# Kernel optimization log

Measured on AMD Instinct MI355X. Metric: run time of the kernel, lower is better.

Reference implementation:

```python
import jax, jax.numpy as jnp
import numpy as np

B, S, D, H, NUM_LABELS = 16, 1024, 1024, 16, 3
LN_EPS = 1e-5


def setup_inputs() -> dict:
    key = jax.random.key(0)
    ks = iter(jax.random.split(key, 16))

    def w(shape, k):
        return jax.random.normal(k, shape, jnp.float32) * 0.02

    inp = {}
    inp["embedded"] = jax.random.normal(next(ks), (B, S, D), jnp.float32)
    inp["attention_mask"] = jnp.ones((B, S), jnp.float32)
    for pfx in ("p2h", "h2p"):
        for name in ("q", "k", "v", "o"):
            inp[f"{pfx}_W{name}"] = w((D, D), next(ks))
            inp[f"{pfx}_b{name}"] = jnp.zeros((D,), jnp.float32)
        inp[f"{pfx}_ln_g"] = jnp.ones((D,), jnp.float32)
        inp[f"{pfx}_ln_b"] = jnp.zeros((D,), jnp.float32)
    inp["W1"] = w((4 * D, D), next(ks)); inp["b1"] = jnp.zeros((D,), jnp.float32)
    inp["W2"] = w((D, D // 2), next(ks)); inp["b2"] = jnp.zeros((D // 2,), jnp.float32)
    inp["W3"] = w((D // 2, NUM_LABELS), next(ks)); inp["b3"] = jnp.zeros((NUM_LABELS,), jnp.float32)
    return inp


def _layernorm(x, g, b):
    mu = jnp.mean(x, axis=-1, keepdims=True)
    var = jnp.mean(jnp.square(x - mu), axis=-1, keepdims=True)
    return (x - mu) / jnp.sqrt(var + LN_EPS) * g + b


def _cross_attn(q_in, kv_in, kv_mask, Wq, bq, Wk, bk, Wv, bv, Wo, bo, g, bln):
    Bs, Sq, Dm = q_in.shape
    Sk = kv_in.shape[1]
    hd = Dm // H
    Q = (q_in @ Wq + bq).reshape(Bs, Sq, H, hd)
    K = (kv_in @ Wk + bk).reshape(Bs, Sk, H, hd)
    V = (kv_in @ Wv + bv).reshape(Bs, Sk, H, hd)
    scores = jnp.einsum("bqhd,bkhd->bhqk", Q, K) / jnp.sqrt(jnp.float32(hd))
    scores = jnp.where(kv_mask[:, None, None, :] == 0, jnp.float32(-1e9), scores)
    wts = jax.nn.softmax(scores, axis=-1)  # dropout is identity in eval
    att = jnp.einsum("bhqk,bkhd->bqhd", wts, V).reshape(Bs, Sq, Dm)
    return _layernorm(att @ Wo + bo + q_in, g, bln)


def _pool(x, m):
    s = jnp.sum(x * m[:, :, None], axis=1)
    d = jnp.clip(jnp.sum(m, axis=1, keepdims=True), 1e-9, None)
    return s / d


def reference(embedded, attention_mask,
              p2h_Wq, p2h_bq, p2h_Wk, p2h_bk, p2h_Wv, p2h_bv, p2h_Wo, p2h_bo, p2h_ln_g, p2h_ln_b,
              h2p_Wq, h2p_bq, h2p_Wk, h2p_bk, h2p_Wv, h2p_bv, h2p_Wo, h2p_bo, h2p_ln_g, h2p_ln_b,
              W1, b1, W2, b2, W3, b3):
    half = embedded.shape[1] // 2
    premise, hypothesis = embedded[:, :half], embedded[:, half:]
    pm, hm = attention_mask[:, :half], attention_mask[:, half:]
    p2h = _cross_attn(premise, hypothesis, hm,
                      p2h_Wq, p2h_bq, p2h_Wk, p2h_bk, p2h_Wv, p2h_bv, p2h_Wo, p2h_bo, p2h_ln_g, p2h_ln_b)
    h2p = _cross_attn(hypothesis, premise, pm,
                      h2p_Wq, h2p_bq, h2p_Wk, h2p_bk, h2p_Wv, h2p_bv, h2p_Wo, h2p_bo, h2p_ln_g, h2p_ln_b)
    feats = jnp.concatenate([_pool(premise, pm), _pool(hypothesis, hm),
                             _pool(p2h, pm), _pool(h2p, hm)], axis=-1)
    h1 = jax.nn.relu(feats @ W1 + b1)
    h2 = jax.nn.relu(h1 @ W2 + b2)
    return h2 @ W3 + b3
```

## Files before the change

kernel.cpp:

```cpp
#include <hip/hip_runtime.h>
#include <hip/hip_bf16.h>

typedef __attribute__((ext_vector_type(8))) __bf16 bf16x8;
typedef __attribute__((ext_vector_type(4))) float f32x4;
typedef __attribute__((ext_vector_type(4))) int i32x4;
typedef __attribute__((ext_vector_type(4))) unsigned short u16x4;

#define MFMA16(a, b, c) __builtin_amdgcn_mfma_f32_16x16x32_bf16((a), (b), (c), 0, 0, 0)

__device__ __forceinline__ void gload_lds16(const void* g, void* l)
{
    __builtin_amdgcn_global_load_lds(
        (const __attribute__((address_space(1))) unsigned int*)g,
        (__attribute__((address_space(3))) unsigned int*)l, 16, 0, 0);
}

__global__ __launch_bounds__(256) void cast_emb_kernel(const float* __restrict__ emb,
                                                       __bf16* __restrict__ Pb,
                                                       __bf16* __restrict__ Hb)
{
    int i = (blockIdx.x * 256 + threadIdx.x) * 4;
    int r = i >> 10, d = i & 1023;
    size_t src = ((size_t)(r >> 9) * 1024 + (r & 511)) * 1024 + d;
    f32x4 p = *(const f32x4*)(emb + src);
    f32x4 h = *(const f32x4*)(emb + src + 512 * 1024);
    union { __bf16 b[4]; u16x4 u; } cp, ch;
#pragma unroll
    for (int j = 0; j < 4; ++j) { cp.b[j] = (__bf16)p[j]; ch.b[j] = (__bf16)h[j]; }
    *(u16x4*)(Pb + i) = cp.u;
    *(u16x4*)(Hb + i) = ch.u;
}

struct WPtrs { const float* p[8]; };
__global__ __launch_bounds__(256) void cast_wt_kernel(WPtrs wp, __bf16* __restrict__ Wt0)
{
    const float* W = wp.p[blockIdx.z];
    __bf16* Wt = Wt0 + (size_t)blockIdx.z * 1048576;
    __shared__ float tile[32][33];
    int n0 = blockIdx.x * 32, k0 = blockIdx.y * 32;
    int tx = threadIdx.x, ty = threadIdx.y;
#pragma unroll
    for (int i = ty; i < 32; i += 8)
        tile[i][tx] = W[(size_t)(k0 + i) * 1024 + n0 + tx];
    __syncthreads();
#pragma unroll
    for (int i = ty; i < 32; i += 8)
        Wt[(size_t)(n0 + i) * 1024 + k0 + tx] = (__bf16)tile[tx][i];
}

template <int EPI>
__global__ __launch_bounds__(256, 3) void gemm_bt(const __bf16* __restrict__ A,
                                                  const __bf16* __restrict__ Bt,
                                                  const float* __restrict__ bias,
                                                  const float* __restrict__ bias2,
                                                  __bf16* __restrict__ Cb,
                                                  __bf16* __restrict__ Cb2,
                                                  float* __restrict__ Cf,
                                                  const float* __restrict__ resid,
                                                  int resid_half, int M, int N, int K)
{
    __shared__ __align__(16) __bf16 As[128 * 32];
    __shared__ __align__(16) __bf16 Bs[128 * 32];
    const int t = threadIdx.x;
    const int l = t & 63, w = t >> 6;
    const int wr = w >> 1, wc = w & 1;
    const int lrow = l & 15, lk = l >> 4;
    const int m0 = blockIdx.y * 128, n0 = blockIdx.x * 128;
    const int r0 = t >> 2, kc0 = (t & 3) * 8;

    const __bf16* gA0 = A + (size_t)(m0 + r0) * K + kc0;
    const __bf16* gA1 = gA0 + (size_t)64 * K;
    const __bf16* gB0 = Bt + (size_t)(n0 + r0) * K + kc0;
    const __bf16* gB1 = gB0 + (size_t)64 * K;
    __bf16* dA0 = &As[r0 * 32 + kc0];
    __bf16* dA1 = &As[(r0 + 64) * 32 + kc0];
    __bf16* dB0 = &Bs[r0 * 32 + kc0];
    __bf16* dB1 = &Bs[(r0 + 64) * 32 + kc0];

    const f32x4 zero = {0.f, 0.f, 0.f, 0.f};
    f32x4 acc[4][4];
#pragma unroll
    for (int mi = 0; mi < 4; ++mi)
#pragma unroll
        for (int ni = 0; ni < 4; ++ni) acc[mi][ni] = zero;

    const int nk = K >> 5;
    for (int kt = 0; kt < nk; ++kt) {
        const int ko = kt * 32;
        gload_lds16(gA0 + ko, dA0);
        gload_lds16(gA1 + ko, dA1);
        gload_lds16(gB0 + ko, dB0);
        gload_lds16(gB1 + ko, dB1);
        __syncthreads();
        bf16x8 af[4], bfv[4];
#pragma unroll
        for (int mi = 0; mi < 4; ++mi)
            af[mi] = *(const bf16x8*)(&As[(wr * 64 + mi * 16 + lrow) * 32 + lk * 8]);
#pragma unroll
        for (int ni = 0; ni < 4; ++ni)
            bfv[ni] = *(const bf16x8*)(&Bs[(wc * 64 + ni * 16 + lrow) * 32 + lk * 8]);
#pragma unroll
        for (int mi = 0; mi < 4; ++mi)
#pragma unroll
            for (int ni = 0; ni < 4; ++ni)
                acc[mi][ni] = MFMA16(af[mi], bfv[ni], acc[mi][ni]);
        __syncthreads();
    }

#pragma unroll
    for (int mi = 0; mi < 4; ++mi) {
#pragma unroll
        for (int ni = 0; ni < 4; ++ni) {
            int col = n0 + wc * 64 + ni * 16 + lrow;
            float bv = (EPI == 3 && col >= 1024) ? bias2[col - 1024] : bias[col];
#pragma unroll
            for (int r = 0; r < 4; ++r) {
                int row = m0 + wr * 64 + mi * 16 + lk * 4 + r;
                float v = acc[mi][ni][r] + bv;
                if (EPI == 0) {
                    Cb[(size_t)row * N + col] = (__bf16)v;
                } else if (EPI == 3) {
                    if (col < 1024) {
                        Cb[(size_t)row * 1024 + col] = (__bf16)v;
                    } else {
                        int c2 = col - 1024;
                        int b_ = row >> 9, pos = row & 511;
                        int h_ = c2 >> 6, hd = c2 & 63;
                        Cb2[(((size_t)(b_ * 16 + h_) * 64 + hd) << 9) + pos] = (__bf16)v;
                    }
                } else {
                    int b_ = row >> 9, s = row & 511;
                    float rv = resid[((size_t)b_ * 1024 + resid_half + s) * 1024 + col];
                    Cf[(size_t)row * N + col] = v + rv;
                }
            }
        }
    }
}

__global__ __launch_bounds__(256, 3) void attn_kernel(const __bf16* __restrict__ Q,
                                                      const __bf16* __restrict__ Kb,
                                                      const __bf16* __restrict__ Vt,
                                                      const float* __restrict__ mask,
                                                      int mask_half,
                                                      __bf16* __restrict__ att)
{
    __shared__ __align__(16) __bf16 KP[256 * 64];
    __shared__ __align__(16) float msk[512];
    const int bh = blockIdx.x, b = bh >> 4, h = bh & 15;
    const int q0 = blockIdx.y * 64;
    const int t = threadIdx.x, l = t & 63, w = t >> 6;
    const int lrow = l & 15, lk = l >> 4;
    char* KPc = (char*)KP;

    const __bf16* kbase = Kb + ((size_t)b * 512) * 1024 + h * 64;
    const __bf16* vsrc = Vt + (size_t)bh * 64 * 512;

#pragma unroll
    for (int i = 0; i < 8; ++i) {
        int c = t + i * 256;
        int pos = c >> 3, gslot = (c & 7) ^ (pos & 7);
        gload_lds16(kbase + (size_t)pos * 1024 + gslot * 8, KPc + c * 16);
    }
    for (int i = t; i < 512; i += 256) msk[i] = mask[b * 1024 + mask_half + i];

    const int qrow = q0 + w * 16 + lrow;
    const __bf16* qptr = Q + ((size_t)(b * 512 + qrow)) * 1024 + h * 64;
    bf16x8 qf0 = *(const bf16x8*)(qptr + lk * 8);
    bf16x8 qf1 = *(const bf16x8*)(qptr + 32 + lk * 8);

    const f32x4 zero = {0.f, 0.f, 0.f, 0.f};
    f32x4 av[4];
#pragma unroll
    for (int ni = 0; ni < 4; ++ni) av[ni] = zero;
    float m_run = -3e38f, su = 0.f;
    const int psw = lrow & 7;
    char* prowp = KPc + (w * 16 + lrow) * 512;
    f32x4 sc[16];

    auto qk_tile = [&]() {
#pragma unroll
        for (int jj = 0; jj < 16; ++jj) {
            const char* kb = KPc + (jj * 16 + lrow) * 128;
            bf16x8 k0 = *(const bf16x8*)(kb + ((lk ^ psw) << 4));
            bf16x8 k1 = *(const bf16x8*)(kb + (((lk + 4) ^ psw) << 4));
            f32x4 c = zero;
            c = MFMA16(k0, qf0, c);
            c = MFMA16(k1, qf1, c);
            sc[jj] = c;
        }
    };

    auto process_tile = [&](int koff) {
        float mt = -3e38f;
#pragma unroll
        for (int jj = 0; jj < 16; ++jj) {
            f32x4 mv = *(const f32x4*)(&msk[koff + jj * 16 + lk * 4]);
#pragma unroll
            for (int r = 0; r < 4; ++r) {
                float s = sc[jj][r] * 0.125f;
                if (mv[r] == 0.f) s = -1e9f;
                sc[jj][r] = s;
                mt = fmaxf(mt, s);
            }
        }
        mt = fmaxf(mt, __shfl_xor(mt, 16));
        mt = fmaxf(mt, __shfl_xor(mt, 32));
        float m_new = fmaxf(m_run, mt);
        float f = __expf(m_run - m_new);
        float ssum = 0.f;
#pragma unroll
        for (int jj = 0; jj < 16; ++jj)
#pragma unroll
            for (int r = 0; r < 4; ++r) {
                float e = __expf(sc[jj][r] - m_new);
                sc[jj][r] = e;
                ssum += e;
            }
        ssum += __shfl_xor(ssum, 16);
        ssum += __shfl_xor(ssum, 32);
        su = su * f + ssum;
        m_run = m_new;
#pragma unroll
        for (int r = 0; r < 4; ++r) {
            float fr = __shfl(f, (l & 48) | (lk * 4 + r));
#pragma unroll
            for (int ni = 0; ni < 4; ++ni) av[ni][r] *= fr;
        }
    };

    auto pv_tile = [&](int koff) {
#pragma unroll
        for (int jj = 0; jj < 16; ++jj) {
            union { __bf16 b[4]; unsigned long long u; } pk;
#pragma unroll
            for (int r = 0; r < 4; ++r) pk.b[r] = (__bf16)sc[jj][r];
            int slot2 = jj * 2 + (lk >> 1);
            *(unsigned long long*)(prowp + (((slot2 ^ psw) << 4) | ((lk & 1) << 3))) = pk.u;
        }
#pragma unroll
        for (int ks = 0; ks < 8; ++ks) {
            bf16x8 pf = *(const bf16x8*)(prowp + (((ks * 4 + lk) ^ psw) << 4));
#pragma unroll
            for (int ni = 0; ni < 4; ++ni) {
                bf16x8 vf = *(const bf16x8*)(&vsrc[(ni * 16 + lrow) * 512 + koff + ks * 32 + lk * 8]);
                av[ni] = MFMA16(pf, vf, av[ni]);
            }
        }
    };

    __syncthreads();
    qk_tile();
    process_tile(0);
    __syncthreads();
    pv_tile(0);
    __syncthreads();
#pragma unroll
    for (int i = 0; i < 8; ++i) {
        int c = t + i * 256;
        int pos = c >> 3, gslot = (c & 7) ^ (pos & 7);
        gload_lds16(kbase + (size_t)(256 + pos) * 1024 + gslot * 8, KPc + c * 16);
    }
    __syncthreads();
    qk_tile();
    process_tile(256);
    __syncthreads();
    pv_tile(256);

    const float inv = 1.f / su;
#pragma unroll
    for (int r = 0; r < 4; ++r) {
        float ivr = __shfl(inv, (l & 48) | (lk * 4 + r));
        int qq = q0 + w * 16 + lk * 4 + r;
#pragma unroll
        for (int ni = 0; ni < 4; ++ni)
            att[((size_t)(b * 512 + qq)) * 1024 + h * 64 + ni * 16 + lrow] =
                (__bf16)(av[ni][r] * ivr);
    }
}

__global__ __launch_bounds__(256) void ln_kernel(const float* __restrict__ X,
                                                 const float* __restrict__ g,
                                                 const float* __restrict__ bta,
                                                 __bf16* __restrict__ out)
{
    const int r = blockIdx.x, t = threadIdx.x;
    const float* x = X + (size_t)r * 1024;
    f32x4 v = *(const f32x4*)(x + t * 4);
    float s = v[0] + v[1] + v[2] + v[3];
    float q = v[0] * v[0] + v[1] * v[1] + v[2] * v[2] + v[3] * v[3];
#pragma unroll
    for (int d = 1; d < 64; d <<= 1) { s += __shfl_xor(s, d); q += __shfl_xor(q, d); }
    __shared__ float rs[4], rq[4];
    if ((t & 63) == 0) { rs[t >> 6] = s; rq[t >> 6] = q; }
    __syncthreads();
    s = rs[0] + rs[1] + rs[2] + rs[3];
    q = rq[0] + rq[1] + rq[2] + rq[3];
    float mu = s * (1.f / 1024.f);
    float var = q * (1.f / 1024.f) - mu * mu;
    float rstd = rsqrtf(var + 1e-5f);
#pragma unroll
    for (int j = 0; j < 4; ++j) {
        int c = t * 4 + j;
        out[(size_t)r * 1024 + c] = (__bf16)((v[j] - mu) * rstd * g[c] + bta[c]);
    }
}

__global__ __launch_bounds__(256) void pool_f32_kernel(const float* __restrict__ X,
                                                       const float* __restrict__ mask,
                                                       float* __restrict__ feats)
{
    const int b = blockIdx.y, d0 = blockIdx.x * 64, half = blockIdx.z * 512;
    const int t = threadIdx.x, d = d0 + (t & 63), sl = t >> 6;
    float acc = 0.f, ms = 0.f;
#pragma unroll 4
    for (int s = sl * 128; s < sl * 128 + 128; ++s) {
        float m = mask[b * 1024 + half + s];
        acc += X[((size_t)b * 1024 + half + s) * 1024 + d] * m;
        ms += m;
    }
    __shared__ float ra[4][64];
    __shared__ float rm[4];
    ra[sl][t & 63] = acc;
    if ((t & 63) == 0) rm[sl] = ms;
    __syncthreads();
    if (t < 64) {
        float a = ra[0][t] + ra[1][t] + ra[2][t] + ra[3][t];
        float m = rm[0] + rm[1] + rm[2] + rm[3];
        feats[b * 4096 + blockIdx.z * 1024 + d0 + t] = a / fmaxf(m, 1e-9f);
    }
}

__global__ __launch_bounds__(256) void pool_bf16_kernel(const __bf16* __restrict__ X,
                                                        const float* __restrict__ mask,
                                                        int half, float* __restrict__ feats,
                                                        int off)
{
    const int b = blockIdx.y, d0 = blockIdx.x * 64;
    const int t = threadIdx.x, d = d0 + (t & 63), sl = t >> 6;
    float acc = 0.f, ms = 0.f;
#pragma unroll 4
    for (int s = sl * 128; s < sl * 128 + 128; ++s) {
        float m = mask[b * 1024 + half + s];
        acc += (float)X[((size_t)b * 512 + s) * 1024 + d] * m;
        ms += m;
    }
    __shared__ float ra[4][64];
    __shared__ float rm[4];
    ra[sl][t & 63] = acc;
    if ((t & 63) == 0) rm[sl] = ms;
    __syncthreads();
    if (t < 64) {
        float a = ra[0][t] + ra[1][t] + ra[2][t] + ra[3][t];
        float m = rm[0] + rm[1] + rm[2] + rm[3];
        feats[b * 4096 + off + d0 + t] = a / fmaxf(m, 1e-9f);
    }
}

__global__ __launch_bounds__(256) void fc_init_kernel(const float* __restrict__ b1,
                                                      const float* __restrict__ b2,
                                                      float* __restrict__ h1,
                                                      float* __restrict__ h2)
{
    int i = blockIdx.x * 256 + threadIdx.x;
    if (i < 16 * 1024) h1[i] = b1[i & 1023];
    else h2[i - 16 * 1024] = b2[(i - 16 * 1024) & 511];
}

template <int CH, int RELU_IN>
__global__ __launch_bounds__(256) void fc_atomic_kernel(const float* __restrict__ in,
                                                        const float* __restrict__ W,
                                                        float* __restrict__ out,
                                                        int IF, int OF)
{
    __shared__ float ins[16 * CH];
    const int t = threadIdx.x;
    const int col = blockIdx.x * 256 + t;
    const int i0 = blockIdx.y * CH;
#pragma unroll
    for (int idx = t; idx < 16 * CH; idx += 256) {
        int b = idx / CH, i = idx % CH;
        float v = in[b * IF + i0 + i];
        if (RELU_IN) v = fmaxf(v, 0.f);
        ins[idx] = v;
    }
    __syncthreads();
    float acc[16];
#pragma unroll
    for (int b = 0; b < 16; ++b) acc[b] = 0.f;
#pragma unroll 4
    for (int i = 0; i < CH; ++i) {
        float wv = W[(size_t)(i0 + i) * OF + col];
#pragma unroll
        for (int b = 0; b < 16; ++b) acc[b] += ins[b * CH + i] * wv;
    }
#pragma unroll
    for (int b = 0; b < 16; ++b) atomicAdd(out + b * OF + col, acc[b]);
}

__global__ __launch_bounds__(64) void mlp3_kernel(const float* __restrict__ h2,
                                                  const float* __restrict__ W3,
                                                  const float* __restrict__ b3,
                                                  float* __restrict__ out)
{
    int b = blockIdx.x, t = threadIdx.x;
    float a0 = 0.f, a1 = 0.f, a2 = 0.f;
    for (int i = t; i < 512; i += 64) {
        float hv = fmaxf(h2[b * 512 + i], 0.f);
        a0 += hv * W3[i * 3 + 0];
        a1 += hv * W3[i * 3 + 1];
        a2 += hv * W3[i * 3 + 2];
    }
#pragma unroll
    for (int d = 1; d < 64; d <<= 1) {
        a0 += __shfl_xor(a0, d);
        a1 += __shfl_xor(a1, d);
        a2 += __shfl_xor(a2, d);
    }
    if (t == 0) {
        out[b * 3 + 0] = a0 + b3[0];
        out[b * 3 + 1] = a1 + b3[1];
        out[b * 3 + 2] = a2 + b3[2];
    }
}

extern "C" void kernel_launch(void* const* d_in, const int* in_sizes, int n_in,
                              void* d_out, int out_size, void* d_ws, size_t ws_size,
                              hipStream_t stream)
{
    const float* emb  = (const float*)d_in[0];
    const float* mask = (const float*)d_in[1];
    const float* W1 = (const float*)d_in[22];
    const float* b1 = (const float*)d_in[23];
    const float* W2 = (const float*)d_in[24];
    const float* b2 = (const float*)d_in[25];
    const float* W3 = (const float*)d_in[26];
    const float* b3 = (const float*)d_in[27];

    char* ws = (char*)d_ws;
    constexpr size_t MB = 1ull << 20;
    __bf16* Pb    = (__bf16*)(ws);
    __bf16* Hb    = (__bf16*)(ws + 16 * MB);
    __bf16* Wt    = (__bf16*)(ws + 32 * MB);
    __bf16* Qb    = (__bf16*)(ws + 48 * MB);
    __bf16* Kb    = (__bf16*)(ws + 64 * MB);
    __bf16* Vt    = (__bf16*)(ws + 80 * MB);
    __bf16* attb  = (__bf16*)(ws + 96 * MB);
    float*  Of    = (float*) (ws + 48 * MB);
    __bf16* ctx   = (__bf16*)(ws + 112 * MB);
    float*  feats = (float*) (ws + 128 * MB);
    float*  h1    = (float*) (ws + 128 * MB + 512 * 1024);
    float*  h2    = (float*) (ws + 129 * MB);

    cast_emb_kernel<<<8192, 256, 0, stream>>>(emb, Pb, Hb);
    WPtrs wp;
    const int widx[8] = {2, 4, 6, 8, 12, 14, 16, 18};
    for (int i = 0; i < 8; ++i) wp.p[i] = (const float*)d_in[widx[i]];
    cast_wt_kernel<<<dim3(32, 32, 8), dim3(32, 8), 0, stream>>>(wp, Wt);

    dim3 gg(8, 64);
    dim3 gkv(16, 64);
    for (int dir = 0; dir < 2; ++dir) {
        const __bf16* qin  = dir ? Hb : Pb;
        const __bf16* kvin = dir ? Pb : Hb;
        const int base = dir ? 12 : 2;
        const __bf16* wq  = Wt + (size_t)(dir * 4 + 0) * 1048576;
        const __bf16* wkv = Wt + (size_t)(dir * 4 + 1) * 1048576;
        const __bf16* wo  = Wt + (size_t)(dir * 4 + 3) * 1048576;
        const float* bq  = (const float*)d_in[base + 1];
        const float* bk  = (const float*)d_in[base + 3];
        const float* bv  = (const float*)d_in[base + 5];
        const float* bo  = (const float*)d_in[base + 7];
        const float* lng = (const float*)d_in[base + 8];
        const float* lnb = (const float*)d_in[base + 9];
        const int kvhalf  = dir ? 0 : 512;
        const int reshalf = dir ? 512 : 0;

        gemm_bt<0><<<gg, 256, 0, stream>>>(qin, wq, bq, nullptr, Qb, nullptr,
                                           nullptr, nullptr, 0, 8192, 1024, 1024);
        gemm_bt<3><<<gkv, 256, 0, stream>>>(kvin, wkv, bk, bv, Kb, Vt,
                                            nullptr, nullptr, 0, 8192, 2048, 1024);
        attn_kernel<<<dim3(256, 8), 256, 0, stream>>>(Qb, Kb, Vt, mask, kvhalf, attb);
        gemm_bt<2><<<gg, 256, 0, stream>>>(attb, wo, bo, nullptr, nullptr, nullptr,
                                           Of, emb, reshalf, 8192, 1024, 1024);
        ln_kernel<<<8192, 256, 0, stream>>>(Of, lng, lnb, ctx);
        pool_bf16_kernel<<<dim3(16, 16), 256, 0, stream>>>(ctx, mask, dir ? 512 : 0,
                                                           feats, 2048 + dir * 1024);
    }
    pool_f32_kernel<<<dim3(16, 16, 2), 256, 0, stream>>>(emb, mask, feats);

    fc_init_kernel<<<96, 256, 0, stream>>>(b1, b2, h1, h2);
    fc_atomic_kernel<128, 0><<<dim3(4, 32), 256, 0, stream>>>(feats, W1, h1, 4096, 1024);
    fc_atomic_kernel<32, 1><<<dim3(2, 32), 256, 0, stream>>>(h1, W2, h2, 1024, 512);
    mlp3_kernel<<<16, 64, 0, stream>>>(h2, W3, b3, (float*)d_out);
}
```

Before: 605.2 us.

## Double-buffer K tiles in attention with smaller 128-key steps and separate P buffer

The attention kernel now walks the 512 keys in four 128-key tiles using two K buffers in LDS. The next tile is prefetched asynchronously while the current one is processed, instead of two serial 256-key phases that share one buffer with the P matrix. This overlaps global loads with compute, halves the score register array, and splits the exp-sum into two accumulators. The GEMM launch bound also drops from 3 to 2 waves-per-EU, which gives more registers at the cost of occupancy. The risk is the extra online-softmax rescaling steps, and the loop's single barrier per tile looks like it could race on the shared P buffer.

```diff
diff --git a/kernel.cpp b/kernel.cpp
--- a/kernel.cpp
+++ b/kernel.cpp
@@ -49,7 +49,7 @@
 }
 
 template <int EPI>
-__global__ __launch_bounds__(256, 3) void gemm_bt(const __bf16* __restrict__ A,
+__global__ __launch_bounds__(256, 2) void gemm_bt(const __bf16* __restrict__ A,
                                                   const __bf16* __restrict__ Bt,
                                                   const float* __restrict__ bias,
                                                   const float* __restrict__ bias2,
@@ -145,24 +145,29 @@
                                                       int mask_half,
                                                       __bf16* __restrict__ att)
 {
-    __shared__ __align__(16) __bf16 KP[256 * 64];
+    __shared__ __align__(16) __bf16 KB[2][128 * 64];
+    __shared__ __align__(16) __bf16 Pt[64 * 128];
     __shared__ __align__(16) float msk[512];
     const int bh = blockIdx.x, b = bh >> 4, h = bh & 15;
     const int q0 = blockIdx.y * 64;
-    const int t = threadIdx.x, l = t & 63, w = t >> 6;
+    const int tid = threadIdx.x, l = tid & 63, w = tid >> 6;
     const int lrow = l & 15, lk = l >> 4;
-    char* KPc = (char*)KP;
 
     const __bf16* kbase = Kb + ((size_t)b * 512) * 1024 + h * 64;
     const __bf16* vsrc = Vt + (size_t)bh * 64 * 512;
 
-#pragma unroll
-    for (int i = 0; i < 8; ++i) {
-        int c = t + i * 256;
-        int pos = c >> 3, gslot = (c & 7) ^ (pos & 7);
-        gload_lds16(kbase + (size_t)pos * 1024 + gslot * 8, KPc + c * 16);
-    }
-    for (int i = t; i < 512; i += 256) msk[i] = mask[b * 1024 + mask_half + i];
+    auto stage = [&](int t, int buf) {
+        char* dst = (char*)KB[buf];
+#pragma unroll
+        for (int i = 0; i < 4; ++i) {
+            int c = tid + i * 256;
+            int pos = c >> 3, gslot = (c & 7) ^ (pos & 7);
+            gload_lds16(kbase + (size_t)(t * 128 + pos) * 1024 + gslot * 8, dst + c * 16);
+        }
+    };
+
+    stage(0, 0);
+    for (int i = tid; i < 512; i += 256) msk[i] = mask[b * 1024 + mask_half + i];
 
     const int qrow = q0 + w * 16 + lrow;
     const __bf16* qptr = Q + ((size_t)(b * 512 + qrow)) * 1024 + h * 64;
@@ -175,13 +180,16 @@
     for (int ni = 0; ni < 4; ++ni) av[ni] = zero;
     float m_run = -3e38f, su = 0.f;
     const int psw = lrow & 7;
-    char* prowp = KPc + (w * 16 + lrow) * 512;
-    f32x4 sc[16];
-
-    auto qk_tile = [&]() {
-#pragma unroll
-        for (int jj = 0; jj < 16; ++jj) {
-            const char* kb = KPc + (jj * 16 + lrow) * 128;
+    char* prowp = (char*)Pt + (w * 16 + lrow) * 256;
+    f32x4 sc[8];
+
+#pragma unroll
+    for (int t = 0; t < 4; ++t) {
+        __syncthreads();
+        const char* kbuf = (const char*)KB[t & 1];
+#pragma unroll
+        for (int jj = 0; jj < 8; ++jj) {
+            const char* kb = kbuf + (jj * 16 + lrow) * 128;
             bf16x8 k0 = *(const bf16x8*)(kb + ((lk ^ psw) << 4));
             bf16x8 k1 = *(const bf16x8*)(kb + (((lk + 4) ^ psw) << 4));
             f32x4 c = zero;
@@ -189,12 +197,12 @@
             c = MFMA16(k1, qf1, c);
             sc[jj] = c;
         }
-    };
-
-    auto process_tile = [&](int koff) {
+        if (t < 3) stage(t + 1, (t + 1) & 1);
+
+        const int koff = t * 128;
         float mt = -3e38f;
 #pragma unroll
-        for (int jj = 0; jj < 16; ++jj) {
+        for (int jj = 0; jj < 8; ++jj) {
             f32x4 mv = *(const f32x4*)(&msk[koff + jj * 16 + lk * 4]);
 #pragma unroll
             for (int r = 0; r < 4; ++r) {
@@ -208,15 +216,18 @@
         mt = fmaxf(mt, __shfl_xor(mt, 32));
         float m_new = fmaxf(m_run, mt);
         float f = __expf(m_run - m_new);
-        float ssum = 0.f;
-#pragma unroll
-        for (int jj = 0; jj < 16; ++jj)
-#pragma unroll
-            for (int r = 0; r < 4; ++r) {
-                float e = __expf(sc[jj][r] - m_new);
-                sc[jj][r] = e;
-                ssum += e;
-            }
+        float s0 = 0.f, s1 = 0.f;
+#pragma unroll
+        for (int jj = 0; jj < 8; ++jj) {
+            float e0 = __expf(sc[jj][0] - m_new);
+            float e1 = __expf(sc[jj][1] - m_new);
+            float e2 = __expf(sc[jj][2] - m_new);
+            float e3 = __expf(sc[jj][3] - m_new);
+            sc[jj][0] = e0; sc[jj][1] = e1; sc[jj][2] = e2; sc[jj][3] = e3;
+            s0 += e0 + e1;
+            s1 += e2 + e3;
+        }
+        float ssum = s0 + s1;
         ssum += __shfl_xor(ssum, 16);
         ssum += __shfl_xor(ssum, 32);
         su = su * f + ssum;
@@ -227,11 +238,9 @@
 #pragma unroll
             for (int ni = 0; ni < 4; ++ni) av[ni][r] *= fr;
         }
-    };
-
-    auto pv_tile = [&](int koff) {
-#pragma unroll
-        for (int jj = 0; jj < 16; ++jj) {
+
+#pragma unroll
+        for (int jj = 0; jj < 8; ++jj) {
             union { __bf16 b[4]; unsigned long long u; } pk;
 #pragma unroll
             for (int r = 0; r < 4; ++r) pk.b[r] = (__bf16)sc[jj][r];
@@ -239,7 +248,7 @@
             *(unsigned long long*)(prowp + (((slot2 ^ psw) << 4) | ((lk & 1) << 3))) = pk.u;
         }
 #pragma unroll
-        for (int ks = 0; ks < 8; ++ks) {
+        for (int ks = 0; ks < 4; ++ks) {
             bf16x8 pf = *(const bf16x8*)(prowp + (((ks * 4 + lk) ^ psw) << 4));
 #pragma unroll
             for (int ni = 0; ni < 4; ++ni) {
@@ -247,25 +256,7 @@
                 av[ni] = MFMA16(pf, vf, av[ni]);
             }
         }
-    };
-
-    __syncthreads();
-    qk_tile();
-    process_tile(0);
-    __syncthreads();
-    pv_tile(0);
-    __syncthreads();
-#pragma unroll
-    for (int i = 0; i < 8; ++i) {
-        int c = t + i * 256;
-        int pos = c >> 3, gslot = (c & 7) ^ (pos & 7);
-        gload_lds16(kbase + (size_t)(256 + pos) * 1024 + gslot * 8, KPc + c * 16);
-    }
-    __syncthreads();
-    qk_tile();
-    process_tile(256);
-    __syncthreads();
-    pv_tile(256);
+    }
 
     const float inv = 1.f / su;
 #pragma unroll
```

Result: no change. 603.4 us (-0.3%).
